# Kernel tuning notes

Hardware: AMD Instinct MI355X
Metric: run time of the kernel (lower is better)

Reference implementation:

```python
import jax, jax.numpy as jnp
import numpy as np

B, S, F = 64, 512, 64      # batch, encoder seq len, input features
H = 512                    # encoder hidden == decoder hidden (required by Attention)
U = 128                    # attention units
T_OUT, OUT_F = 96, 1       # output horizon, output features


def _p(key, shape, scale=0.05):
    return scale * jax.random.normal(key, shape, dtype=jnp.float32)


def setup_inputs() -> dict:
    key = jax.random.key(0)
    ks = jax.random.split(key, 18)
    d = {
        "x": jax.random.normal(ks[0], (B, S, F), dtype=jnp.float32),
        # encoder LSTM (torch gate order i,f,g,o)
        "enc_Wih": _p(ks[1], (4 * H, F)),
        "enc_Whh": _p(ks[2], (4 * H, H)),
        "enc_bih": _p(ks[3], (4 * H,)),
        "enc_bhh": _p(ks[4], (4 * H,)),
        # attention
        "att_W1": _p(ks[5], (U, H)),
        "att_b1": _p(ks[6], (U,)),
        "att_W2": _p(ks[7], (U, H)),
        "att_b2": _p(ks[8], (U,)),
        "att_V": _p(ks[9], (1, U)),
        "att_bV": _p(ks[10], (1,)),
        # decoder LSTM: input = cat(context[H], y_t[OUT_F])
        "dec_Wih": _p(ks[11], (4 * H, H + OUT_F)),
        "dec_Whh": _p(ks[12], (4 * H, H)),
        "dec_bih": _p(ks[13], (4 * H,)),
        "dec_bhh": _p(ks[14], (4 * H,)),
        # output projection
        "out_W": _p(ks[15], (OUT_F, H)),
        "out_b": _p(ks[16], (OUT_F,)),
    }
    return d


def _lstm_gates(pre):
    i, f, g, o = jnp.split(pre, 4, axis=-1)
    return jax.nn.sigmoid(i), jax.nn.sigmoid(f), jnp.tanh(g), jax.nn.sigmoid(o)


def _forward(x, enc_Wih, enc_Whh, enc_bih, enc_bhh,
             att_W1, att_b1, att_W2, att_b2, att_V, att_bV,
             dec_Wih, dec_Whh, dec_bih, dec_bhh, out_W, out_b):
    b = x.shape[0]
    # ---- encoder LSTM over S steps ----
    x_pre = jnp.einsum('bsf,gf->bsg', x, enc_Wih) + enc_bih + enc_bhh  # precompute input GEMM

    def enc_step(carry, xp_t):
        h, c = carry
        i, f, g, o = _lstm_gates(xp_t + h @ enc_Whh.T)
        c = f * c + i * g
        h = o * jnp.tanh(c)
        return (h, c), h

    h0 = jnp.zeros((b, H), x.dtype)
    (enc_hn, _), enc_out = jax.lax.scan(enc_step, (h0, h0), jnp.swapaxes(x_pre, 0, 1))
    enc_out = jnp.swapaxes(enc_out, 0, 1)  # [B,S,H]

    # W2(enc_out) is step-invariant -> hoist out of the decode loop
    w2_enc = jnp.einsum('bsh,uh->bsu', enc_out, att_W2) + att_b2  # [B,S,U]

    # y is None in inference path -> teacher-forcing inputs are zeros
    y_t = jnp.zeros((b, OUT_F), x.dtype)
    dec_bias = dec_bih + dec_bhh  # h0=c0=0 each decoder call (torch code passes no state)

    def dec_step(h_att, _):
        # Bahdanau attention
        w1_h = h_att @ att_W1.T + att_b1                       # [B,U]
        score = jnp.tanh(w1_h[:, None, :] + w2_enc) @ att_V.T + att_bV  # [B,S,1]
        attn = jax.nn.softmax(score, axis=1)
        ctx = jnp.sum(attn * enc_out, axis=1)                  # [B,H]
        # single decoder LSTM cell step from zero state
        x_t = jnp.concatenate([ctx, y_t], axis=-1)             # [B,H+OUT_F]
        i, f, g, o = _lstm_gates(x_t @ dec_Wih.T + dec_bias)   # f*c0 = 0, Whh@h0 = 0
        c = i * g
        h = o * jnp.tanh(c)
        out_t = h @ out_W.T + out_b                            # [B,OUT_F]
        return h, out_t

    _, outs = jax.lax.scan(dec_step, enc_hn, None, length=T_OUT)
    return jnp.swapaxes(outs, 0, 1)  # [B,T_OUT,OUT_F]


def reference(x, enc_Wih, enc_Whh, enc_bih, enc_bhh,
              att_W1, att_b1, att_W2, att_b2, att_V, att_bV,
              dec_Wih, dec_Whh, dec_bih, dec_bhh, out_W, out_b):
    return _forward(x, enc_Wih, enc_Whh, enc_bih, enc_bhh,
                    att_W1, att_b1, att_W2, att_b2, att_V, att_bV,
                    dec_Wih, dec_Whh, dec_bih, dec_bhh, out_W, out_b)
```

## Files before the change

kernel.cpp:

```cpp
#include <hip/hip_runtime.h>

#define Bn 64
#define Sn 512
#define Fn 64
#define Hn 512
#define Un 128
#define Tn 96

typedef __attribute__((ext_vector_type(8))) short bf16x8;
typedef __attribute__((ext_vector_type(4))) float f32x4;

#define MFMA16(a, b, c) __builtin_amdgcn_mfma_f32_16x16x32_bf16(a, b, c, 0, 0, 0)

__device__ __forceinline__ float sigm(float x) { return 1.0f / (1.0f + __expf(-x)); }
__device__ __forceinline__ float tanh_f(float x) {
    x = fminf(fmaxf(x, -15.0f), 15.0f);
    float e = __expf(2.0f * x);
    return (e - 1.0f) / (e + 1.0f);
}
__device__ __forceinline__ short bf16rtn(float f) {
    unsigned u = __float_as_uint(f);
    unsigned r = (u + 0x7FFFu + ((u >> 16) & 1u)) >> 16;
    return (short)r;
}
__device__ __forceinline__ float bf16tof(short s) {
    return __uint_as_float(((unsigned)(unsigned short)s) << 16);
}

__global__ __launch_bounds__(256) void k_split_x(const float* __restrict__ x,
                                                 short* __restrict__ xhi, short* __restrict__ xlo) {
    int t = blockIdx.x * 256 + threadIdx.x;
    int f = t & 63, s = (t >> 6) & 511, b = t >> 15;
    float v = x[t];
    short hi = bf16rtn(v);
    short lo = bf16rtn(v - bf16tof(hi));
    int o = (s * Bn + b) * Fn + f;
    xhi[o] = hi; xlo[o] = lo;
}
__global__ __launch_bounds__(256) void k_split_whh(const float* __restrict__ w,
                                                   short* __restrict__ whi, short* __restrict__ wlo) {
    int t = blockIdx.x * 256 + threadIdx.x;
    int k = t & 511, r = t >> 9;
    int g = r >> 9, j = r & 511;
    float v = w[t];
    short hi = bf16rtn(v);
    short lo = bf16rtn(v - bf16tof(hi));
    int o = (j * 4 + g) * 512 + k;
    whi[o] = hi; wlo[o] = lo;
}
__global__ __launch_bounds__(256) void k_split_wih(const float* __restrict__ w,
                                                   short* __restrict__ whi, short* __restrict__ wlo) {
    int t = blockIdx.x * 256 + threadIdx.x;
    int k = t & 63, r = t >> 6;
    int g = r >> 9, j = r & 511;
    float v = w[t];
    short hi = bf16rtn(v);
    short lo = bf16rtn(v - bf16tof(hi));
    int o = (j * 4 + g) * 64 + k;
    whi[o] = hi; wlo[o] = lo;
}
__global__ __launch_bounds__(256) void k_bias_perm(const float* __restrict__ bih,
                                                   const float* __restrict__ bhh,
                                                   float* __restrict__ bperm) {
    int t = blockIdx.x * 256 + threadIdx.x;
    int g = t >> 9, j = t & 511;
    bperm[j * 4 + g] = bih[t] + bhh[t];
}
__global__ __launch_bounds__(256) void k_w1t(const float* __restrict__ W1, float* __restrict__ W1T) {
    int t = blockIdx.x * 256 + threadIdx.x;
    int u = t >> 9, k = t & 511;
    W1T[k * Un + u] = W1[t];
}
__global__ __launch_bounds__(256) void k_w2t_bf16(const float* __restrict__ W2, short* __restrict__ W2Tb) {
    int t = blockIdx.x * 256 + threadIdx.x;
    int u = t >> 9, j = t & 511;
    W2Tb[j * Un + u] = bf16rtn(W2[t]);
}
__global__ __launch_bounds__(256) void k_transpose_dec(const float* __restrict__ dW, float* __restrict__ WiT,
                                                       float* __restrict__ WgT, float* __restrict__ WoT) {
    int t = blockIdx.x * 256 + threadIdx.x;
    int j = t & 511, j2 = t >> 9;
    WiT[t] = dW[(j)        * 513 + j2];
    WgT[t] = dW[(1024 + j) * 513 + j2];
    WoT[t] = dW[(1536 + j) * 513 + j2];
}
__global__ __launch_bounds__(256) void k_zero_state(float* __restrict__ hz, float* __restrict__ se) {
    int t = blockIdx.x * 256 + threadIdx.x;
    if (t < 98304) hz[t] = 0.0f;
    else se[t - 98304] = 0.0f;
}

__global__ __launch_bounds__(256)
void enc_step_mfma(const short* __restrict__ xhi, const short* __restrict__ xlo,
                   const short* __restrict__ whhHi, const short* __restrict__ whhLo,
                   const short* __restrict__ wihHi, const short* __restrict__ wihLo,
                   const float* __restrict__ bperm,
                   const short* __restrict__ hHiP, const short* __restrict__ hLoP,
                   short* __restrict__ hHiN, short* __restrict__ hLoN,
                   float* __restrict__ cstG, short* __restrict__ encJ, int t)
{
    const int blk = blockIdx.x;
    const int jt = blk >> 2, bt = blk & 3;
    const int tid = threadIdx.x;
    const int wv = tid >> 6, l = tid & 63;
    const int lr = l & 15, lk = l >> 4;
    const int row  = jt * 16 + lr;
    const int bcol = bt * 16 + lr;

    f32x4 acc0 = {0.f, 0.f, 0.f, 0.f};
    f32x4 acc1 = {0.f, 0.f, 0.f, 0.f};
    #pragma unroll
    for (int c = 0; c < 4; c++) {
        int k0 = wv * 128 + c * 32 + lk * 8;
        bf16x8 Ah = *(const bf16x8*)(whhHi + row * 512 + k0);
        bf16x8 Al = *(const bf16x8*)(whhLo + row * 512 + k0);
        bf16x8 Bh = *(const bf16x8*)(hHiP + bcol * 512 + k0);
        bf16x8 Bl = *(const bf16x8*)(hLoP + bcol * 512 + k0);
        if (c & 1) {
            acc1 = MFMA16(Ah, Bh, acc1);
            acc1 = MFMA16(Ah, Bl, acc1);
            acc1 = MFMA16(Al, Bh, acc1);
        } else {
            acc0 = MFMA16(Ah, Bh, acc0);
            acc0 = MFMA16(Ah, Bl, acc0);
            acc0 = MFMA16(Al, Bh, acc0);
        }
    }
    if (wv < 2) {
        int k0 = wv * 32 + lk * 8;
        bf16x8 Ah = *(const bf16x8*)(wihHi + row * 64 + k0);
        bf16x8 Al = *(const bf16x8*)(wihLo + row * 64 + k0);
        bf16x8 Bh = *(const bf16x8*)(xhi + ((size_t)t * 64 + bcol) * 64 + k0);
        bf16x8 Bl = *(const bf16x8*)(xlo + ((size_t)t * 64 + bcol) * 64 + k0);
        acc0 = MFMA16(Ah, Bh, acc0);
        acc1 = MFMA16(Ah, Bl, acc1);
        acc0 = MFMA16(Al, Bh, acc0);
    }
    f32x4 acc = acc0 + acc1;

    __shared__ float red[3][64][4];
    if (wv) *(f32x4*)(&red[wv - 1][l][0]) = acc;
    __syncthreads();
    if (wv == 0) {
        const int jloc = jt * 4 + lk;
        const f32x4 bias = *(const f32x4*)(bperm + jt * 16 + lk * 4);
        f32x4 r0 = *(const f32x4*)(&red[0][l][0]);
        f32x4 r1 = *(const f32x4*)(&red[1][l][0]);
        f32x4 r2 = *(const f32x4*)(&red[2][l][0]);
        float pi = acc[0] + r0[0] + r1[0] + r2[0] + bias[0];
        float pf = acc[1] + r0[1] + r1[1] + r2[1] + bias[1];
        float pg = acc[2] + r0[2] + r1[2] + r2[2] + bias[2];
        float po = acc[3] + r0[3] + r1[3] + r2[3] + bias[3];
        float ig = sigm(pi), fg = sigm(pf), gg = tanh_f(pg), og = sigm(po);
        float cn = fg * cstG[jloc * Bn + bcol] + ig * gg;
        float hv = og * tanh_f(cn);
        cstG[jloc * Bn + bcol] = cn;
        short hi16 = bf16rtn(hv);
        short lo16 = bf16rtn(hv - bf16tof(hi16));
        hHiN[bcol * 512 + jloc] = hi16;
        hLoN[bcol * 512 + jloc] = lo16;
        encJ[jloc * (Sn * Bn) + t * Bn + bcol] = hi16;
    }
}

__global__ __launch_bounds__(256)
void w2enc_k(const short* __restrict__ encJ, const short* __restrict__ W2Tb,
             const float* __restrict__ b2, short* __restrict__ w2eb)
{
    __shared__ float tile[64 * 64];
    const int s = blockIdx.x;
    const int tid = threadIdx.x;
    const int u = tid & 127, bq = tid >> 7;
    float acc[32];
    #pragma unroll
    for (int i = 0; i < 32; i++) acc[i] = 0.f;
    for (int jc = 0; jc < 8; jc++) {
        __syncthreads();
        #pragma unroll
        for (int r = 0; r < 16; r++) {
            int e = r * 256 + tid;
            int jl = e >> 6, b = e & 63;
            tile[e] = bf16tof(encJ[(jc * 64 + jl) * (Sn * Bn) + s * Bn + b]);
        }
        __syncthreads();
        for (int jl = 0; jl < 64; jl++) {
            float wv = bf16tof(W2Tb[(jc * 64 + jl) * Un + u]);
            const float4* trow = (const float4*)&tile[jl * 64 + bq * 32];
            #pragma unroll
            for (int i = 0; i < 8; i++) {
                float4 t4 = trow[i];
                acc[i*4+0] += t4.x * wv; acc[i*4+1] += t4.y * wv;
                acc[i*4+2] += t4.z * wv; acc[i*4+3] += t4.w * wv;
            }
        }
    }
    float bb = b2[u];
    #pragma unroll
    for (int i = 0; i < 32; i++)
        w2eb[(((size_t)(bq * 32 + i)) * Sn + s) * Un + u] = bf16rtn(acc[i] + bb);
}

__global__ __launch_bounds__(256)
void dec_attn_k(const float* __restrict__ hdec, const short* __restrict__ encJ,
                const float* __restrict__ W1T, const float* __restrict__ b1,
                const float* __restrict__ Vv, const float* __restrict__ bV,
                const short* __restrict__ w2eb, const float* __restrict__ oW,
                const float* __restrict__ ob, float* __restrict__ eT,
                float* __restrict__ sumE, float* __restrict__ out, int t)
{
    __shared__ float hs[512];
    __shared__ float w1h[Un];
    __shared__ float Vs[Un];
    __shared__ float red2[256];
    const int tid = threadIdx.x;
    const int b = blockIdx.x >> 2, sc = blockIdx.x & 3;

    if (t == 0) {
        hs[tid]       = bf16tof(encJ[tid * (Sn * Bn) + (Sn - 1) * Bn + b]);
        hs[tid + 256] = bf16tof(encJ[(tid + 256) * (Sn * Bn) + (Sn - 1) * Bn + b]);
    } else {
        hs[tid]       = hdec[tid * Bn + b];
        hs[tid + 256] = hdec[(tid + 256) * Bn + b];
    }
    if (tid < 128) Vs[tid] = Vv[tid];
    __syncthreads();

    if (sc == 0 && t > 0) {
        red2[tid] = oW[tid] * hs[tid] + oW[tid + 256] * hs[tid + 256];
        __syncthreads();
        for (int w = 128; w > 0; w >>= 1) { if (tid < w) red2[tid] += red2[tid + w]; __syncthreads(); }
        if (tid == 0) out[b * Tn + (t - 1)] = red2[0] + ob[0];
        __syncthreads();
    }

    {
        const int u = tid & 127, kh = tid >> 7;
        float a = 0.f;
        #pragma unroll 8
        for (int k = 0; k < 256; k++) {
            int kk = kh * 256 + k;
            a += W1T[kk * Un + u] * hs[kk];
        }
        red2[tid] = a;
    }
    __syncthreads();
    if (tid < 128) w1h[tid] = red2[tid] + red2[tid + 128] + b1[tid];
    __syncthreads();

    const int sl = sc * 128 + (tid >> 1), uh = tid & 1;
    const short* r  = w2eb + ((size_t)b * Sn + sl) * Un + uh * 64;
    const float* wp = w1h + uh * 64;
    const float* vp = Vs + uh * 64;
    float s0 = 0.f;
    #pragma unroll 4
    for (int u2 = 0; u2 < 64; u2++) s0 += vp[u2] * tanh_f(wp[u2] + bf16tof(r[u2]));
    s0 += __shfl_xor(s0, 1);
    float e = 0.f;
    if (uh == 0) {
        e = __expf(s0 + bV[0]);
        eT[sl * Bn + b] = e;
    }
    __syncthreads();
    red2[tid] = e;
    __syncthreads();
    for (int w = 128; w > 0; w >>= 1) { if (tid < w) red2[tid] += red2[tid + w]; __syncthreads(); }
    if (tid == 0) atomicAdd(&sumE[t * Bn + b], red2[0]);
}

__global__ __launch_bounds__(256)
void dec_ctx_k(const float* __restrict__ eT, const short* __restrict__ encJ,
               float* __restrict__ ctx)
{
    const int tid = threadIdx.x;
    const int j = blockIdx.x;
    const int b = tid & 63, sq = tid >> 6;
    const short* ep = encJ + j * (Sn * Bn) + b;
    float a = 0.f;
    #pragma unroll 8
    for (int s = sq * 128; s < sq * 128 + 128; s++)
        a += eT[s * Bn + b] * bf16tof(ep[s * Bn]);
    __shared__ float red[256];
    red[tid] = a;
    __syncthreads();
    if (sq == 0) ctx[j * Bn + b] = red[b] + red[64 + b] + red[128 + b] + red[192 + b];
}

__global__ __launch_bounds__(256)
void dec_gate_k(const float* __restrict__ ctx, const float* __restrict__ sumE,
                const float* __restrict__ WiT, const float* __restrict__ WgT,
                const float* __restrict__ WoT, const float* __restrict__ dbih,
                const float* __restrict__ dbhh, float* __restrict__ hdec, int t)
{
    const int tid = threadIdx.x;
    const int b = tid & 63, kq = tid >> 6;
    const int j = blockIdx.x;
    float ai = 0.f, ag = 0.f, ao = 0.f;
    #pragma unroll 4
    for (int k = kq * 128; k < kq * 128 + 128; k++) {
        float cv = ctx[k * Bn + b];
        ai += WiT[k * Hn + j] * cv;
        ag += WgT[k * Hn + j] * cv;
        ao += WoT[k * Hn + j] * cv;
    }
    __shared__ float red[3][4][64];
    red[0][kq][b] = ai; red[1][kq][b] = ag; red[2][kq][b] = ao;
    __syncthreads();
    if (kq == 0) {
        float inv = 1.0f / sumE[t * Bn + b];
        float pi = (red[0][0][b] + red[0][1][b] + red[0][2][b] + red[0][3][b]) * inv + dbih[j] + dbhh[j];
        float pg = (red[1][0][b] + red[1][1][b] + red[1][2][b] + red[1][3][b]) * inv + dbih[2*Hn + j] + dbhh[2*Hn + j];
        float po = (red[2][0][b] + red[2][1][b] + red[2][2][b] + red[2][3][b]) * inv + dbih[3*Hn + j] + dbhh[3*Hn + j];
        float cc = sigm(pi) * tanh_f(pg);
        float hh = sigm(po) * tanh_f(cc);
        hdec[j * Bn + b] = hh;
    }
}

__global__ __launch_bounds__(64)
void dec_out_k(const float* __restrict__ hdec, const float* __restrict__ oW,
               const float* __restrict__ ob, float* __restrict__ out, int t)
{
    const int b = blockIdx.x;
    const int tid = threadIdx.x;
    float a = 0.f;
    #pragma unroll
    for (int q = 0; q < 8; q++) {
        int j = tid + q * 64;
        a += oW[j] * hdec[j * Bn + b];
    }
    for (int off = 32; off; off >>= 1) a += __shfl_down(a, off, 64);
    if (tid == 0) out[b * Tn + t] = a + ob[0];
}

extern "C" void kernel_launch(void* const* d_in, const int* in_sizes, int n_in,
                              void* d_out, int out_size, void* d_ws, size_t ws_size,
                              hipStream_t stream) {
    const float* x    = (const float*)d_in[0];
    const float* eWih = (const float*)d_in[1];
    const float* eWhh = (const float*)d_in[2];
    const float* ebih = (const float*)d_in[3];
    const float* ebhh = (const float*)d_in[4];
    const float* aW1  = (const float*)d_in[5];
    const float* ab1  = (const float*)d_in[6];
    const float* aW2  = (const float*)d_in[7];
    const float* ab2  = (const float*)d_in[8];
    const float* aV   = (const float*)d_in[9];
    const float* abV  = (const float*)d_in[10];
    const float* dWih = (const float*)d_in[11];
    const float* dbih = (const float*)d_in[13];
    const float* dbhh = (const float*)d_in[14];
    const float* oW   = (const float*)d_in[15];
    const float* ob   = (const float*)d_in[16];
    float* out = (float*)d_out;

    char* wsb = (char*)d_ws;
    short* xhi    = (short*)(wsb + 0);
    short* xlo    = (short*)(wsb + 4194304);
    short* whhHi  = (short*)(wsb + 8388608);
    short* whhLo  = (short*)(wsb + 10485760);
    short* wihHi  = (short*)(wsb + 12582912);
    short* wihLo  = (short*)(wsb + 12845056);
    float* bperm  = (float*)(wsb + 13107200);
    short* W2Tb   = (short*)(wsb + 13115392);
    float* W1T    = (float*)(wsb + 13246464);
    float* WiT    = (float*)(wsb + 13508608);
    float* WgT    = (float*)(wsb + 14557184);
    float* WoT    = (float*)(wsb + 15605760);
    short* hHi    = (short*)(wsb + 16654336);
    short* hLo    = (short*)(wsb + 16785408);
    float* cstG   = (float*)(wsb + 16916480);
    short* encJ   = (short*)(wsb + 17047552);
    short* w2eb   = (short*)(wsb + 50601984);
    float* eT     = (float*)(wsb + 58990592);
    float* sumE   = (float*)(wsb + 59121664);
    float* ctx    = (float*)(wsb + 59146240);
    float* hdec   = (float*)(wsb + 59277312);

    k_split_x      <<<8192, 256, 0, stream>>>(x, xhi, xlo);
    k_split_whh    <<<4096, 256, 0, stream>>>(eWhh, whhHi, whhLo);
    k_split_wih    <<<512,  256, 0, stream>>>(eWih, wihHi, wihLo);
    k_bias_perm    <<<8,    256, 0, stream>>>(ebih, ebhh, bperm);
    k_w1t          <<<256,  256, 0, stream>>>(aW1, W1T);
    k_w2t_bf16     <<<256,  256, 0, stream>>>(aW2, W2Tb);
    k_transpose_dec<<<1024, 256, 0, stream>>>(dWih, WiT, WgT, WoT);
    k_zero_state   <<<408,  256, 0, stream>>>((float*)hHi, sumE);

    for (int t = 0; t < Sn; t++) {
        const int pr = t & 1, pw = 1 - pr;
        enc_step_mfma<<<512, 256, 0, stream>>>(xhi, xlo, whhHi, whhLo, wihHi, wihLo,
                                               bperm,
                                               hHi + pr * 32768, hLo + pr * 32768,
                                               hHi + pw * 32768, hLo + pw * 32768,
                                               cstG, encJ, t);
    }

    w2enc_k<<<512, 256, 0, stream>>>(encJ, W2Tb, ab2, w2eb);

    for (int t = 0; t < Tn; t++) {
        dec_attn_k<<<256, 256, 0, stream>>>(hdec, encJ, W1T, ab1, aV, abV, w2eb,
                                            oW, ob, eT, sumE, out, t);
        dec_ctx_k <<<512, 256, 0, stream>>>(eT, encJ, ctx);
        dec_gate_k<<<512, 256, 0, stream>>>(ctx, sumE, WiT, WgT, WoT, dbih, dbhh, hdec, t);
    }
    dec_out_k<<<64, 64, 0, stream>>>(hdec, oW, ob, out, Tn - 1);
}
```

Before: 7.694 ms.

## Fuse encoder time loop into persistent kernel with global atomic barrier

Replaces 512 per-timestep encoder kernel launches with one persistent kernel that loops over time, keeping Whh/Wih fragments and cell state in registers. Steps are separated by a grid-wide barrier built from spread atomic counters with spin-waiting, and the hi/lo bf16 hidden halves are packed into one u32 so each element is exchanged with a single relaxed atomic store. This removes launch overhead and repeated weight reloads, but it depends on all 512 blocks being co-resident (launch bounds 256,2) and on relaxed atomics giving correct visibility; spin latency could also dominate.

```diff
diff --git a/kernel.cpp b/kernel.cpp
--- a/kernel.cpp
+++ b/kernel.cpp
@@ -9,6 +9,8 @@
 
 typedef __attribute__((ext_vector_type(8))) short bf16x8;
 typedef __attribute__((ext_vector_type(4))) float f32x4;
+typedef unsigned int u32;
+typedef unsigned long long u64;
 
 #define MFMA16(a, b, c) __builtin_amdgcn_mfma_f32_16x16x32_bf16(a, b, c, 0, 0, 0)
 
@@ -84,20 +86,19 @@
     WgT[t] = dW[(1024 + j) * 513 + j2];
     WoT[t] = dW[(1536 + j) * 513 + j2];
 }
-__global__ __launch_bounds__(256) void k_zero_state(float* __restrict__ hz, float* __restrict__ se) {
-    int t = blockIdx.x * 256 + threadIdx.x;
-    if (t < 98304) hz[t] = 0.0f;
-    else se[t - 98304] = 0.0f;
-}
-
-__global__ __launch_bounds__(256)
-void enc_step_mfma(const short* __restrict__ xhi, const short* __restrict__ xlo,
-                   const short* __restrict__ whhHi, const short* __restrict__ whhLo,
-                   const short* __restrict__ wihHi, const short* __restrict__ wihLo,
-                   const float* __restrict__ bperm,
-                   const short* __restrict__ hHiP, const short* __restrict__ hLoP,
-                   short* __restrict__ hHiN, short* __restrict__ hLoN,
-                   float* __restrict__ cstG, short* __restrict__ encJ, int t)
+__global__ __launch_bounds__(256) void k_zero_state(u32* __restrict__ z, float* __restrict__ se) {
+    int t = blockIdx.x * 256 + threadIdx.x;
+    if (t < 131072) z[t] = 0u;
+    else se[t - 131072] = 0.0f;
+}
+
+__global__ __launch_bounds__(256, 2)
+void enc_persist2(const short* __restrict__ xhi, const short* __restrict__ xlo,
+                  const short* __restrict__ whhHi, const short* __restrict__ whhLo,
+                  const short* __restrict__ wihHi, const short* __restrict__ wihLo,
+                  const float* __restrict__ bperm,
+                  u32* __restrict__ hPk, u32* __restrict__ ctrs,
+                  short* __restrict__ encJ)
 {
     const int blk = blockIdx.x;
     const int jt = blk >> 2, bt = blk & 3;
@@ -107,59 +108,104 @@
     const int row  = jt * 16 + lr;
     const int bcol = bt * 16 + lr;
 
-    f32x4 acc0 = {0.f, 0.f, 0.f, 0.f};
-    f32x4 acc1 = {0.f, 0.f, 0.f, 0.f};
+    bf16x8 Ahi[4], Alo[4];
     #pragma unroll
     for (int c = 0; c < 4; c++) {
         int k0 = wv * 128 + c * 32 + lk * 8;
-        bf16x8 Ah = *(const bf16x8*)(whhHi + row * 512 + k0);
-        bf16x8 Al = *(const bf16x8*)(whhLo + row * 512 + k0);
-        bf16x8 Bh = *(const bf16x8*)(hHiP + bcol * 512 + k0);
-        bf16x8 Bl = *(const bf16x8*)(hLoP + bcol * 512 + k0);
-        if (c & 1) {
-            acc1 = MFMA16(Ah, Bh, acc1);
-            acc1 = MFMA16(Ah, Bl, acc1);
-            acc1 = MFMA16(Al, Bh, acc1);
-        } else {
-            acc0 = MFMA16(Ah, Bh, acc0);
-            acc0 = MFMA16(Ah, Bl, acc0);
-            acc0 = MFMA16(Al, Bh, acc0);
-        }
-    }
+        Ahi[c] = *(const bf16x8*)(whhHi + row * 512 + k0);
+        Alo[c] = *(const bf16x8*)(whhLo + row * 512 + k0);
+    }
+    bf16x8 AXhi = {}, AXlo = {};
     if (wv < 2) {
         int k0 = wv * 32 + lk * 8;
-        bf16x8 Ah = *(const bf16x8*)(wihHi + row * 64 + k0);
-        bf16x8 Al = *(const bf16x8*)(wihLo + row * 64 + k0);
-        bf16x8 Bh = *(const bf16x8*)(xhi + ((size_t)t * 64 + bcol) * 64 + k0);
-        bf16x8 Bl = *(const bf16x8*)(xlo + ((size_t)t * 64 + bcol) * 64 + k0);
-        acc0 = MFMA16(Ah, Bh, acc0);
-        acc1 = MFMA16(Ah, Bl, acc1);
-        acc0 = MFMA16(Al, Bh, acc0);
-    }
-    f32x4 acc = acc0 + acc1;
+        AXhi = *(const bf16x8*)(wihHi + row * 64 + k0);
+        AXlo = *(const bf16x8*)(wihLo + row * 64 + k0);
+    }
+    const int jloc = jt * 4 + lk;
+    const int bV   = bt * 16 + lr;
+    const f32x4 bias = *(const f32x4*)(bperm + jt * 16 + lk * 4);
+    float cst = 0.0f;
 
     __shared__ float red[3][64][4];
-    if (wv) *(f32x4*)(&red[wv - 1][l][0]) = acc;
-    __syncthreads();
-    if (wv == 0) {
-        const int jloc = jt * 4 + lk;
-        const f32x4 bias = *(const f32x4*)(bperm + jt * 16 + lk * 4);
-        f32x4 r0 = *(const f32x4*)(&red[0][l][0]);
-        f32x4 r1 = *(const f32x4*)(&red[1][l][0]);
-        f32x4 r2 = *(const f32x4*)(&red[2][l][0]);
-        float pi = acc[0] + r0[0] + r1[0] + r2[0] + bias[0];
-        float pf = acc[1] + r0[1] + r1[1] + r2[1] + bias[1];
-        float pg = acc[2] + r0[2] + r1[2] + r2[2] + bias[2];
-        float po = acc[3] + r0[3] + r1[3] + r2[3] + bias[3];
-        float ig = sigm(pi), fg = sigm(pf), gg = tanh_f(pg), og = sigm(po);
-        float cn = fg * cstG[jloc * Bn + bcol] + ig * gg;
-        float hv = og * tanh_f(cn);
-        cstG[jloc * Bn + bcol] = cn;
-        short hi16 = bf16rtn(hv);
-        short lo16 = bf16rtn(hv - bf16tof(hi16));
-        hHiN[bcol * 512 + jloc] = hi16;
-        hLoN[bcol * 512 + jloc] = lo16;
-        encJ[jloc * (Sn * Bn) + t * Bn + bcol] = hi16;
+
+    #pragma unroll 1
+    for (int t = 0; t < 512; t++) {
+        const int pr = t & 1;
+        const u32* hp = hPk + pr * 32768 + bcol * 512;
+        f32x4 acc0 = {0.f, 0.f, 0.f, 0.f};
+        f32x4 acc1 = {0.f, 0.f, 0.f, 0.f};
+        #pragma unroll
+        for (int c = 0; c < 4; c++) {
+            int k0 = wv * 128 + c * 32 + lk * 8;
+            const u64* q = (const u64*)(hp + k0);
+            union { u64 q[4]; u32 d[8]; } u;
+            u.q[0] = __hip_atomic_load(q + 0, __ATOMIC_RELAXED, __HIP_MEMORY_SCOPE_AGENT);
+            u.q[1] = __hip_atomic_load(q + 1, __ATOMIC_RELAXED, __HIP_MEMORY_SCOPE_AGENT);
+            u.q[2] = __hip_atomic_load(q + 2, __ATOMIC_RELAXED, __HIP_MEMORY_SCOPE_AGENT);
+            u.q[3] = __hip_atomic_load(q + 3, __ATOMIC_RELAXED, __HIP_MEMORY_SCOPE_AGENT);
+            union { bf16x8 v; u32 d[4]; } Bh, Bl;
+            #pragma unroll
+            for (int i = 0; i < 4; i++) {
+                u32 a = u.d[2 * i], b = u.d[2 * i + 1];
+                Bh.d[i] = (a >> 16) | (b & 0xFFFF0000u);
+                Bl.d[i] = (a & 0xFFFFu) | (b << 16);
+            }
+            if (c & 1) {
+                acc1 = MFMA16(Ahi[c], Bh.v, acc1);
+                acc1 = MFMA16(Ahi[c], Bl.v, acc1);
+                acc1 = MFMA16(Alo[c], Bh.v, acc1);
+            } else {
+                acc0 = MFMA16(Ahi[c], Bh.v, acc0);
+                acc0 = MFMA16(Ahi[c], Bl.v, acc0);
+                acc0 = MFMA16(Alo[c], Bh.v, acc0);
+            }
+        }
+        if (wv < 2) {
+            int k0 = wv * 32 + lk * 8;
+            bf16x8 Bh = *(const bf16x8*)(xhi + ((size_t)t * 64 + bcol) * 64 + k0);
+            bf16x8 Bl = *(const bf16x8*)(xlo + ((size_t)t * 64 + bcol) * 64 + k0);
+            acc0 = MFMA16(AXhi, Bh, acc0);
+            acc1 = MFMA16(AXhi, Bl, acc1);
+            acc0 = MFMA16(AXlo, Bh, acc0);
+        }
+        f32x4 acc = acc0 + acc1;
+
+        if (wv) *(f32x4*)(&red[wv - 1][l][0]) = acc;
+        __syncthreads();
+        if (wv == 0) {
+            f32x4 r0 = *(const f32x4*)(&red[0][l][0]);
+            f32x4 r1 = *(const f32x4*)(&red[1][l][0]);
+            f32x4 r2 = *(const f32x4*)(&red[2][l][0]);
+            float pi = acc[0] + r0[0] + r1[0] + r2[0] + bias[0];
+            float pf = acc[1] + r0[1] + r1[1] + r2[1] + bias[1];
+            float pg = acc[2] + r0[2] + r1[2] + r2[2] + bias[2];
+            float po = acc[3] + r0[3] + r1[3] + r2[3] + bias[3];
+            float ig = sigm(pi), fg = sigm(pf), gg = tanh_f(pg), og = sigm(po);
+            cst = fg * cst + ig * gg;
+            float hv = og * tanh_f(cst);
+            short hi16 = bf16rtn(hv);
+            short lo16 = bf16rtn(hv - bf16tof(hi16));
+            u32 pk = ((u32)(unsigned short)hi16 << 16) | (u32)(unsigned short)lo16;
+            __hip_atomic_store(hPk + (1 - pr) * 32768 + bV * 512 + jloc, pk,
+                               __ATOMIC_RELAXED, __HIP_MEMORY_SCOPE_AGENT);
+            encJ[jloc * (Sn * Bn) + t * Bn + bV] = hi16;
+        }
+        asm volatile("s_waitcnt vmcnt(0)" ::: "memory");
+        if (tid == 0) {
+            u32* cb = ctrs + t * 128;
+            __hip_atomic_fetch_add(cb + (blk & 7) * 16, 1u,
+                                   __ATOMIC_RELAXED, __HIP_MEMORY_SCOPE_AGENT);
+            u32 sum;
+            do {
+                sum = 0u;
+                #pragma unroll
+                for (int i = 0; i < 8; i++)
+                    sum += __hip_atomic_load(cb + i * 16, __ATOMIC_RELAXED,
+                                             __HIP_MEMORY_SCOPE_AGENT);
+                if (sum < 512u) __builtin_amdgcn_s_sleep(1);
+            } while (sum < 512u);
+        }
+        __syncthreads();
     }
 }
 
@@ -366,15 +412,14 @@
     float* WiT    = (float*)(wsb + 13508608);
     float* WgT    = (float*)(wsb + 14557184);
     float* WoT    = (float*)(wsb + 15605760);
-    short* hHi    = (short*)(wsb + 16654336);
-    short* hLo    = (short*)(wsb + 16785408);
-    float* cstG   = (float*)(wsb + 16916480);
-    short* encJ   = (short*)(wsb + 17047552);
-    short* w2eb   = (short*)(wsb + 50601984);
-    float* eT     = (float*)(wsb + 58990592);
-    float* sumE   = (float*)(wsb + 59121664);
-    float* ctx    = (float*)(wsb + 59146240);
-    float* hdec   = (float*)(wsb + 59277312);
+    u32*   hPk    = (u32*)  (wsb + 16654336);
+    u32*   ctrs   = (u32*)  (wsb + 16916480);
+    short* encJ   = (short*)(wsb + 17178624);
+    short* w2eb   = (short*)(wsb + 50733056);
+    float* eT     = (float*)(wsb + 59121664);
+    float* sumE   = (float*)(wsb + 59252736);
+    float* ctx    = (float*)(wsb + 59277312);
+    float* hdec   = (float*)(wsb + 59408384);
 
     k_split_x      <<<8192, 256, 0, stream>>>(x, xhi, xlo);
     k_split_whh    <<<4096, 256, 0, stream>>>(eWhh, whhHi, whhLo);
@@ -383,16 +428,10 @@
     k_w1t          <<<256,  256, 0, stream>>>(aW1, W1T);
     k_w2t_bf16     <<<256,  256, 0, stream>>>(aW2, W2Tb);
     k_transpose_dec<<<1024, 256, 0, stream>>>(dWih, WiT, WgT, WoT);
-    k_zero_state   <<<408,  256, 0, stream>>>((float*)hHi, sumE);
-
-    for (int t = 0; t < Sn; t++) {
-        const int pr = t & 1, pw = 1 - pr;
-        enc_step_mfma<<<512, 256, 0, stream>>>(xhi, xlo, whhHi, whhLo, wihHi, wihLo,
-                                               bperm,
-                                               hHi + pr * 32768, hLo + pr * 32768,
-                                               hHi + pw * 32768, hLo + pw * 32768,
-                                               cstG, encJ, t);
-    }
+    k_zero_state   <<<536,  256, 0, stream>>>(hPk, sumE);
+
+    enc_persist2<<<512, 256, 0, stream>>>(xhi, xlo, whhHi, whhLo, wihHi, wihLo,
+                                          bperm, hPk, ctrs, encJ);
 
     w2enc_k<<<512, 256, 0, stream>>>(encJ, W2Tb, ab2, w2eb);
 
```

New measurement: 11.75 ms. 1.53x slower.

## Replace per-step encoder launches with persistent kernel using global flag barrier

Applied to the files above, without the earlier changes.

Swaps the 512 per-timestep encoder kernel launches for a single persistent 32-block kernel. Each block owns 64 gate rows, keeps its cell state in registers and reads packed hi/lo hidden state through agent-scope atomic loads into LDS. Blocks then synchronize across steps with a spin-wait flag barrier, which removes launch overhead and the cross-wave LDS reduction. It also vectorizes the bf16 loads in the attention score loop. The cost is that only 32 CUs are used, each block re-reads its weight rows every step, and the design depends on all blocks being co-resident and on relaxed-atomic visibility being correct.

```diff
diff --git a/kernel.cpp b/kernel.cpp
--- a/kernel.cpp
+++ b/kernel.cpp
@@ -9,8 +9,11 @@
 
 typedef __attribute__((ext_vector_type(8))) short bf16x8;
 typedef __attribute__((ext_vector_type(4))) float f32x4;
+typedef unsigned int u32;
+typedef unsigned long long u64;
 
 #define MFMA16(a, b, c) __builtin_amdgcn_mfma_f32_16x16x32_bf16(a, b, c, 0, 0, 0)
+#define ALOAD64(p) __hip_atomic_load((p), __ATOMIC_RELAXED, __HIP_MEMORY_SCOPE_AGENT)
 
 __device__ __forceinline__ float sigm(float x) { return 1.0f / (1.0f + __expf(-x)); }
 __device__ __forceinline__ float tanh_f(float x) {
@@ -84,82 +87,158 @@
     WgT[t] = dW[(1024 + j) * 513 + j2];
     WoT[t] = dW[(1536 + j) * 513 + j2];
 }
-__global__ __launch_bounds__(256) void k_zero_state(float* __restrict__ hz, float* __restrict__ se) {
-    int t = blockIdx.x * 256 + threadIdx.x;
-    if (t < 98304) hz[t] = 0.0f;
-    else se[t - 98304] = 0.0f;
-}
-
-__global__ __launch_bounds__(256)
-void enc_step_mfma(const short* __restrict__ xhi, const short* __restrict__ xlo,
-                   const short* __restrict__ whhHi, const short* __restrict__ whhLo,
-                   const short* __restrict__ wihHi, const short* __restrict__ wihLo,
-                   const float* __restrict__ bperm,
-                   const short* __restrict__ hHiP, const short* __restrict__ hLoP,
-                   short* __restrict__ hHiN, short* __restrict__ hLoN,
-                   float* __restrict__ cstG, short* __restrict__ encJ, int t)
-{
+__global__ __launch_bounds__(256) void k_zero_state(u32* __restrict__ z, float* __restrict__ se) {
+    int t = blockIdx.x * 256 + threadIdx.x;
+    if (t < 66048) z[t] = 0u;
+    else se[t - 66048] = 0.0f;
+}
+
+__global__ __launch_bounds__(256, 1)
+void enc_persist3(const short* __restrict__ xhi, const short* __restrict__ xlo,
+                  const short* __restrict__ whhHi, const short* __restrict__ whhLo,
+                  const short* __restrict__ wihHi, const short* __restrict__ wihLo,
+                  const float* __restrict__ bperm,
+                  u32* __restrict__ hPk, u32* __restrict__ flags,
+                  short* __restrict__ encJ)
+{
+    __shared__ short hiL[64 * 520];
+    __shared__ short loL[64 * 520];
     const int blk = blockIdx.x;
-    const int jt = blk >> 2, bt = blk & 3;
     const int tid = threadIdx.x;
     const int wv = tid >> 6, l = tid & 63;
     const int lr = l & 15, lk = l >> 4;
-    const int row  = jt * 16 + lr;
-    const int bcol = bt * 16 + lr;
-
-    f32x4 acc0 = {0.f, 0.f, 0.f, 0.f};
-    f32x4 acc1 = {0.f, 0.f, 0.f, 0.f};
+    const int rtB = (wv >> 1) * 32;
+    const int ctB = (wv & 1) * 32;
+    const int r0 = blk * 64 + rtB + lr;
+    const int r1 = r0 + 16;
+    const int b0 = ctB + lr, b1 = b0 + 16;
+
+    bf16x8 XA[2][2][2];
     #pragma unroll
-    for (int c = 0; c < 4; c++) {
-        int k0 = wv * 128 + c * 32 + lk * 8;
-        bf16x8 Ah = *(const bf16x8*)(whhHi + row * 512 + k0);
-        bf16x8 Al = *(const bf16x8*)(whhLo + row * 512 + k0);
-        bf16x8 Bh = *(const bf16x8*)(hHiP + bcol * 512 + k0);
-        bf16x8 Bl = *(const bf16x8*)(hLoP + bcol * 512 + k0);
-        if (c & 1) {
-            acc1 = MFMA16(Ah, Bh, acc1);
-            acc1 = MFMA16(Ah, Bl, acc1);
-            acc1 = MFMA16(Al, Bh, acc1);
-        } else {
-            acc0 = MFMA16(Ah, Bh, acc0);
-            acc0 = MFMA16(Ah, Bl, acc0);
-            acc0 = MFMA16(Al, Bh, acc0);
-        }
-    }
-    if (wv < 2) {
-        int k0 = wv * 32 + lk * 8;
-        bf16x8 Ah = *(const bf16x8*)(wihHi + row * 64 + k0);
-        bf16x8 Al = *(const bf16x8*)(wihLo + row * 64 + k0);
-        bf16x8 Bh = *(const bf16x8*)(xhi + ((size_t)t * 64 + bcol) * 64 + k0);
-        bf16x8 Bl = *(const bf16x8*)(xlo + ((size_t)t * 64 + bcol) * 64 + k0);
-        acc0 = MFMA16(Ah, Bh, acc0);
-        acc1 = MFMA16(Ah, Bl, acc1);
-        acc0 = MFMA16(Al, Bh, acc0);
-    }
-    f32x4 acc = acc0 + acc1;
-
-    __shared__ float red[3][64][4];
-    if (wv) *(f32x4*)(&red[wv - 1][l][0]) = acc;
-    __syncthreads();
-    if (wv == 0) {
-        const int jloc = jt * 4 + lk;
-        const f32x4 bias = *(const f32x4*)(bperm + jt * 16 + lk * 4);
-        f32x4 r0 = *(const f32x4*)(&red[0][l][0]);
-        f32x4 r1 = *(const f32x4*)(&red[1][l][0]);
-        f32x4 r2 = *(const f32x4*)(&red[2][l][0]);
-        float pi = acc[0] + r0[0] + r1[0] + r2[0] + bias[0];
-        float pf = acc[1] + r0[1] + r1[1] + r2[1] + bias[1];
-        float pg = acc[2] + r0[2] + r1[2] + r2[2] + bias[2];
-        float po = acc[3] + r0[3] + r1[3] + r2[3] + bias[3];
-        float ig = sigm(pi), fg = sigm(pf), gg = tanh_f(pg), og = sigm(po);
-        float cn = fg * cstG[jloc * Bn + bcol] + ig * gg;
-        float hv = og * tanh_f(cn);
-        cstG[jloc * Bn + bcol] = cn;
-        short hi16 = bf16rtn(hv);
-        short lo16 = bf16rtn(hv - bf16tof(hi16));
-        hHiN[bcol * 512 + jloc] = hi16;
-        hLoN[bcol * 512 + jloc] = lo16;
-        encJ[jloc * (Sn * Bn) + t * Bn + bcol] = hi16;
+    for (int cw = 0; cw < 2; cw++) {
+        int k0 = cw * 32 + lk * 8;
+        XA[cw][0][0] = *(const bf16x8*)(wihHi + r0 * 64 + k0);
+        XA[cw][0][1] = *(const bf16x8*)(wihLo + r0 * 64 + k0);
+        XA[cw][1][0] = *(const bf16x8*)(wihHi + r1 * 64 + k0);
+        XA[cw][1][1] = *(const bf16x8*)(wihLo + r1 * 64 + k0);
+    }
+    const f32x4 bias0 = *(const f32x4*)(bperm + blk * 64 + rtB + lk * 4);
+    const f32x4 bias1 = *(const f32x4*)(bperm + blk * 64 + rtB + 16 + lk * 4);
+    float cst[2][2] = {{0.f, 0.f}, {0.f, 0.f}};
+
+    #pragma unroll 1
+    for (int t = 0; t < 512; t++) {
+        const int pr = t & 1;
+        bf16x8 XB[2][2][2];
+        #pragma unroll
+        for (int cw = 0; cw < 2; cw++) {
+            int k0 = cw * 32 + lk * 8;
+            XB[cw][0][0] = *(const bf16x8*)(xhi + ((size_t)t * 64 + b0) * 64 + k0);
+            XB[cw][0][1] = *(const bf16x8*)(xlo + ((size_t)t * 64 + b0) * 64 + k0);
+            XB[cw][1][0] = *(const bf16x8*)(xhi + ((size_t)t * 64 + b1) * 64 + k0);
+            XB[cw][1][1] = *(const bf16x8*)(xlo + ((size_t)t * 64 + b1) * 64 + k0);
+        }
+        {
+            const u32* src = hPk + pr * 32768;
+            #pragma unroll 4
+            for (int i = 0; i < 16; i++) {
+                int idx = i * 2048 + tid * 8;
+                const u64* q = (const u64*)(src + idx);
+                u64 q0 = ALOAD64(q + 0);
+                u64 q1 = ALOAD64(q + 1);
+                u64 q2 = ALOAD64(q + 2);
+                u64 q3 = ALOAD64(q + 3);
+                u32 d0 = (u32)q0, d1 = (u32)(q0 >> 32);
+                u32 d2 = (u32)q1, d3 = (u32)(q1 >> 32);
+                u32 d4 = (u32)q2, d5 = (u32)(q2 >> 32);
+                u32 d6 = (u32)q3, d7 = (u32)(q3 >> 32);
+                union { bf16x8 v; u32 d[4]; } H, L;
+                H.d[0] = (d0 >> 16) | (d1 & 0xFFFF0000u);
+                L.d[0] = (d0 & 0xFFFFu) | (d1 << 16);
+                H.d[1] = (d2 >> 16) | (d3 & 0xFFFF0000u);
+                L.d[1] = (d2 & 0xFFFFu) | (d3 << 16);
+                H.d[2] = (d4 >> 16) | (d5 & 0xFFFF0000u);
+                L.d[2] = (d4 & 0xFFFFu) | (d5 << 16);
+                H.d[3] = (d6 >> 16) | (d7 & 0xFFFF0000u);
+                L.d[3] = (d6 & 0xFFFFu) | (d7 << 16);
+                int bb = idx >> 9, kk = idx & 511;
+                *(bf16x8*)(&hiL[bb * 520 + kk]) = H.v;
+                *(bf16x8*)(&loL[bb * 520 + kk]) = L.v;
+            }
+        }
+        __syncthreads();
+        f32x4 a00 = {0.f,0.f,0.f,0.f}, a01 = {0.f,0.f,0.f,0.f};
+        f32x4 a10 = {0.f,0.f,0.f,0.f}, a11 = {0.f,0.f,0.f,0.f};
+        #pragma unroll 4
+        for (int c = 0; c < 16; c++) {
+            int k0 = c * 32 + lk * 8;
+            bf16x8 Ah0 = *(const bf16x8*)(whhHi + (size_t)r0 * 512 + k0);
+            bf16x8 Al0 = *(const bf16x8*)(whhLo + (size_t)r0 * 512 + k0);
+            bf16x8 Ah1 = *(const bf16x8*)(whhHi + (size_t)r1 * 512 + k0);
+            bf16x8 Al1 = *(const bf16x8*)(whhLo + (size_t)r1 * 512 + k0);
+            bf16x8 Bh0 = *(const bf16x8*)(&hiL[b0 * 520 + k0]);
+            bf16x8 Bl0 = *(const bf16x8*)(&loL[b0 * 520 + k0]);
+            bf16x8 Bh1 = *(const bf16x8*)(&hiL[b1 * 520 + k0]);
+            bf16x8 Bl1 = *(const bf16x8*)(&loL[b1 * 520 + k0]);
+            a00 = MFMA16(Ah0, Bh0, a00); a00 = MFMA16(Ah0, Bl0, a00); a00 = MFMA16(Al0, Bh0, a00);
+            a01 = MFMA16(Ah0, Bh1, a01); a01 = MFMA16(Ah0, Bl1, a01); a01 = MFMA16(Al0, Bh1, a01);
+            a10 = MFMA16(Ah1, Bh0, a10); a10 = MFMA16(Ah1, Bl0, a10); a10 = MFMA16(Al1, Bh0, a10);
+            a11 = MFMA16(Ah1, Bh1, a11); a11 = MFMA16(Ah1, Bl1, a11); a11 = MFMA16(Al1, Bh1, a11);
+        }
+        #pragma unroll
+        for (int cw = 0; cw < 2; cw++) {
+            a00 = MFMA16(XA[cw][0][0], XB[cw][0][0], a00);
+            a00 = MFMA16(XA[cw][0][0], XB[cw][0][1], a00);
+            a00 = MFMA16(XA[cw][0][1], XB[cw][0][0], a00);
+            a01 = MFMA16(XA[cw][0][0], XB[cw][1][0], a01);
+            a01 = MFMA16(XA[cw][0][0], XB[cw][1][1], a01);
+            a01 = MFMA16(XA[cw][0][1], XB[cw][1][0], a01);
+            a10 = MFMA16(XA[cw][1][0], XB[cw][0][0], a10);
+            a10 = MFMA16(XA[cw][1][0], XB[cw][0][1], a10);
+            a10 = MFMA16(XA[cw][1][1], XB[cw][0][0], a10);
+            a11 = MFMA16(XA[cw][1][0], XB[cw][1][0], a11);
+            a11 = MFMA16(XA[cw][1][0], XB[cw][1][1], a11);
+            a11 = MFMA16(XA[cw][1][1], XB[cw][1][0], a11);
+        }
+        const int pw = 1 - pr;
+        #pragma unroll
+        for (int i = 0; i < 2; i++) {
+            #pragma unroll
+            for (int j = 0; j < 2; j++) {
+                f32x4 A = (i == 0) ? ((j == 0) ? a00 : a01) : ((j == 0) ? a10 : a11);
+                f32x4 bs = (i == 0) ? bias0 : bias1;
+                float pi = A[0] + bs[0];
+                float pf = A[1] + bs[1];
+                float pg = A[2] + bs[2];
+                float po = A[3] + bs[3];
+                float ig = sigm(pi), fg = sigm(pf), gg = tanh_f(pg), og = sigm(po);
+                float cn = fg * cst[i][j] + ig * gg;
+                cst[i][j] = cn;
+                float hv = og * tanh_f(cn);
+                short hi16 = bf16rtn(hv);
+                short lo16 = bf16rtn(hv - bf16tof(hi16));
+                u32 pk = ((u32)(unsigned short)hi16 << 16) | (u32)(unsigned short)lo16;
+                int jg = blk * 16 + (wv >> 1) * 8 + i * 4 + lk;
+                int bb = ctB + j * 16 + lr;
+                __hip_atomic_store(hPk + pw * 32768 + bb * 512 + jg, pk,
+                                   __ATOMIC_RELAXED, __HIP_MEMORY_SCOPE_AGENT);
+                encJ[(size_t)jg * (Sn * Bn) + t * 64 + bb] = hi16;
+            }
+        }
+        __syncthreads();
+        if (tid == 0)
+            __hip_atomic_store(&flags[blk * 16], (u32)(t + 1),
+                               __ATOMIC_RELAXED, __HIP_MEMORY_SCOPE_AGENT);
+        if (wv == 0) {
+            while (true) {
+                u32 v = (l < 32) ? __hip_atomic_load(&flags[l * 16], __ATOMIC_RELAXED,
+                                                     __HIP_MEMORY_SCOPE_AGENT)
+                                 : 0xFFFFFFFFu;
+                if (__all(v > (u32)t)) break;
+                __builtin_amdgcn_s_sleep(2);
+            }
+        }
+        __syncthreads();
     }
 }
 
@@ -252,8 +331,13 @@
     const float* wp = w1h + uh * 64;
     const float* vp = Vs + uh * 64;
     float s0 = 0.f;
-    #pragma unroll 4
-    for (int u2 = 0; u2 < 64; u2++) s0 += vp[u2] * tanh_f(wp[u2] + bf16tof(r[u2]));
+    #pragma unroll
+    for (int q = 0; q < 8; q++) {
+        bf16x8 v8 = *(const bf16x8*)(r + q * 8);
+        #pragma unroll
+        for (int e2 = 0; e2 < 8; e2++)
+            s0 += vp[q * 8 + e2] * tanh_f(wp[q * 8 + e2] + bf16tof(v8[e2]));
+    }
     s0 += __shfl_xor(s0, 1);
     float e = 0.f;
     if (uh == 0) {
@@ -366,15 +450,14 @@
     float* WiT    = (float*)(wsb + 13508608);
     float* WgT    = (float*)(wsb + 14557184);
     float* WoT    = (float*)(wsb + 15605760);
-    short* hHi    = (short*)(wsb + 16654336);
-    short* hLo    = (short*)(wsb + 16785408);
-    float* cstG   = (float*)(wsb + 16916480);
-    short* encJ   = (short*)(wsb + 17047552);
-    short* w2eb   = (short*)(wsb + 50601984);
-    float* eT     = (float*)(wsb + 58990592);
-    float* sumE   = (float*)(wsb + 59121664);
-    float* ctx    = (float*)(wsb + 59146240);
-    float* hdec   = (float*)(wsb + 59277312);
+    u32*   hPk    = (u32*)  (wsb + 16654336);
+    u32*   flags  = (u32*)  (wsb + 16916480);
+    short* encJ   = (short*)(wsb + 16918528);
+    short* w2eb   = (short*)(wsb + 50472960);
+    float* eT     = (float*)(wsb + 58861568);
+    float* sumE   = (float*)(wsb + 58992640);
+    float* ctx    = (float*)(wsb + 59017216);
+    float* hdec   = (float*)(wsb + 59148288);
 
     k_split_x      <<<8192, 256, 0, stream>>>(x, xhi, xlo);
     k_split_whh    <<<4096, 256, 0, stream>>>(eWhh, whhHi, whhLo);
@@ -383,16 +466,10 @@
     k_w1t          <<<256,  256, 0, stream>>>(aW1, W1T);
     k_w2t_bf16     <<<256,  256, 0, stream>>>(aW2, W2Tb);
     k_transpose_dec<<<1024, 256, 0, stream>>>(dWih, WiT, WgT, WoT);
-    k_zero_state   <<<408,  256, 0, stream>>>((float*)hHi, sumE);
-
-    for (int t = 0; t < Sn; t++) {
-        const int pr = t & 1, pw = 1 - pr;
-        enc_step_mfma<<<512, 256, 0, stream>>>(xhi, xlo, whhHi, whhLo, wihHi, wihLo,
-                                               bperm,
-                                               hHi + pr * 32768, hLo + pr * 32768,
-                                               hHi + pw * 32768, hLo + pw * 32768,
-                                               cstG, encJ, t);
-    }
+    k_zero_state   <<<282,  256, 0, stream>>>(hPk, sumE);
+
+    enc_persist3<<<32, 256, 0, stream>>>(xhi, xlo, whhHi, whhLo, wihHi, wihLo,
+                                         bperm, hPk, flags, encJ);
 
     w2enc_k<<<512, 256, 0, stream>>>(encJ, W2Tb, ab2, w2eb);
 
```

Result: slower. 11.94 ms (+55.2%).

## Restructure encoder step to one block per gate tile with full-K per wave

Applied to the files above, without the earlier changes.

The encoder step kernel drops from 512 blocks, where each block split K across four waves and reduced through shared memory, to 128 blocks where each wave owns a 16-column batch tile and runs the full K=512 loop itself. This removes the shared-memory reduction and the __syncthreads, and each block loads the Whh row tile once for all four batch tiles. The cost is a longer serial MFMA chain per wave with a single accumulator and fewer blocks on the GPU. The attention score loop also switches to vectorized 8-wide bf16 loads of the w2enc row.

```diff
diff --git a/kernel.cpp b/kernel.cpp
--- a/kernel.cpp
+++ b/kernel.cpp
@@ -9,6 +9,7 @@
 
 typedef __attribute__((ext_vector_type(8))) short bf16x8;
 typedef __attribute__((ext_vector_type(4))) float f32x4;
+typedef unsigned int u32;
 
 #define MFMA16(a, b, c) __builtin_amdgcn_mfma_f32_16x16x32_bf16(a, b, c, 0, 0, 0)
 
@@ -91,76 +92,66 @@
 }
 
 __global__ __launch_bounds__(256)
-void enc_step_mfma(const short* __restrict__ xhi, const short* __restrict__ xlo,
-                   const short* __restrict__ whhHi, const short* __restrict__ whhLo,
-                   const short* __restrict__ wihHi, const short* __restrict__ wihLo,
-                   const float* __restrict__ bperm,
-                   const short* __restrict__ hHiP, const short* __restrict__ hLoP,
-                   short* __restrict__ hHiN, short* __restrict__ hLoN,
-                   float* __restrict__ cstG, short* __restrict__ encJ, int t)
-{
-    const int blk = blockIdx.x;
-    const int jt = blk >> 2, bt = blk & 3;
+void enc_step2(const short* __restrict__ xhi, const short* __restrict__ xlo,
+               const short* __restrict__ whhHi, const short* __restrict__ whhLo,
+               const short* __restrict__ wihHi, const short* __restrict__ wihLo,
+               const float* __restrict__ bperm,
+               const short* __restrict__ hHiP, const short* __restrict__ hLoP,
+               short* __restrict__ hHiN, short* __restrict__ hLoN,
+               float* __restrict__ cstG, short* __restrict__ encJ, int t)
+{
+    const int jt = blockIdx.x;
     const int tid = threadIdx.x;
     const int wv = tid >> 6, l = tid & 63;
     const int lr = l & 15, lk = l >> 4;
     const int row  = jt * 16 + lr;
-    const int bcol = bt * 16 + lr;
-
-    f32x4 acc0 = {0.f, 0.f, 0.f, 0.f};
-    f32x4 acc1 = {0.f, 0.f, 0.f, 0.f};
-    #pragma unroll
-    for (int c = 0; c < 4; c++) {
-        int k0 = wv * 128 + c * 32 + lk * 8;
-        bf16x8 Ah = *(const bf16x8*)(whhHi + row * 512 + k0);
-        bf16x8 Al = *(const bf16x8*)(whhLo + row * 512 + k0);
-        bf16x8 Bh = *(const bf16x8*)(hHiP + bcol * 512 + k0);
-        bf16x8 Bl = *(const bf16x8*)(hLoP + bcol * 512 + k0);
-        if (c & 1) {
-            acc1 = MFMA16(Ah, Bh, acc1);
-            acc1 = MFMA16(Ah, Bl, acc1);
-            acc1 = MFMA16(Al, Bh, acc1);
-        } else {
-            acc0 = MFMA16(Ah, Bh, acc0);
-            acc0 = MFMA16(Ah, Bl, acc0);
-            acc0 = MFMA16(Al, Bh, acc0);
+    const int bcol = wv * 16 + lr;
+
+    f32x4 acc = {0.f, 0.f, 0.f, 0.f};
+    {
+        bf16x8 XB[2][2];
+        #pragma unroll
+        for (int cw = 0; cw < 2; cw++) {
+            int k0 = cw * 32 + lk * 8;
+            XB[cw][0] = *(const bf16x8*)(xhi + ((size_t)t * 64 + bcol) * 64 + k0);
+            XB[cw][1] = *(const bf16x8*)(xlo + ((size_t)t * 64 + bcol) * 64 + k0);
         }
-    }
-    if (wv < 2) {
-        int k0 = wv * 32 + lk * 8;
-        bf16x8 Ah = *(const bf16x8*)(wihHi + row * 64 + k0);
-        bf16x8 Al = *(const bf16x8*)(wihLo + row * 64 + k0);
-        bf16x8 Bh = *(const bf16x8*)(xhi + ((size_t)t * 64 + bcol) * 64 + k0);
-        bf16x8 Bl = *(const bf16x8*)(xlo + ((size_t)t * 64 + bcol) * 64 + k0);
-        acc0 = MFMA16(Ah, Bh, acc0);
-        acc1 = MFMA16(Ah, Bl, acc1);
-        acc0 = MFMA16(Al, Bh, acc0);
-    }
-    f32x4 acc = acc0 + acc1;
-
-    __shared__ float red[3][64][4];
-    if (wv) *(f32x4*)(&red[wv - 1][l][0]) = acc;
-    __syncthreads();
-    if (wv == 0) {
-        const int jloc = jt * 4 + lk;
-        const f32x4 bias = *(const f32x4*)(bperm + jt * 16 + lk * 4);
-        f32x4 r0 = *(const f32x4*)(&red[0][l][0]);
-        f32x4 r1 = *(const f32x4*)(&red[1][l][0]);
-        f32x4 r2 = *(const f32x4*)(&red[2][l][0]);
-        float pi = acc[0] + r0[0] + r1[0] + r2[0] + bias[0];
-        float pf = acc[1] + r0[1] + r1[1] + r2[1] + bias[1];
-        float pg = acc[2] + r0[2] + r1[2] + r2[2] + bias[2];
-        float po = acc[3] + r0[3] + r1[3] + r2[3] + bias[3];
-        float ig = sigm(pi), fg = sigm(pf), gg = tanh_f(pg), og = sigm(po);
-        float cn = fg * cstG[jloc * Bn + bcol] + ig * gg;
-        float hv = og * tanh_f(cn);
-        cstG[jloc * Bn + bcol] = cn;
-        short hi16 = bf16rtn(hv);
-        short lo16 = bf16rtn(hv - bf16tof(hi16));
-        hHiN[bcol * 512 + jloc] = hi16;
-        hLoN[bcol * 512 + jloc] = lo16;
-        encJ[jloc * (Sn * Bn) + t * Bn + bcol] = hi16;
-    }
+        #pragma unroll
+        for (int cw = 0; cw < 2; cw++) {
+            int k0 = cw * 32 + lk * 8;
+            bf16x8 Ah = *(const bf16x8*)(wihHi + (size_t)row * 64 + k0);
+            bf16x8 Al = *(const bf16x8*)(wihLo + (size_t)row * 64 + k0);
+            acc = MFMA16(Ah, XB[cw][0], acc);
+            acc = MFMA16(Ah, XB[cw][1], acc);
+            acc = MFMA16(Al, XB[cw][0], acc);
+        }
+    }
+    #pragma unroll 4
+    for (int c = 0; c < 16; c++) {
+        int k0 = c * 32 + lk * 8;
+        bf16x8 Ah = *(const bf16x8*)(whhHi + (size_t)row * 512 + k0);
+        bf16x8 Al = *(const bf16x8*)(whhLo + (size_t)row * 512 + k0);
+        bf16x8 Bh = *(const bf16x8*)(hHiP + (size_t)bcol * 512 + k0);
+        bf16x8 Bl = *(const bf16x8*)(hLoP + (size_t)bcol * 512 + k0);
+        acc = MFMA16(Ah, Bh, acc);
+        acc = MFMA16(Ah, Bl, acc);
+        acc = MFMA16(Al, Bh, acc);
+    }
+    const int jloc = jt * 4 + lk;
+    const f32x4 bias = *(const f32x4*)(bperm + jt * 16 + lk * 4);
+    float pi = acc[0] + bias[0];
+    float pf = acc[1] + bias[1];
+    float pg = acc[2] + bias[2];
+    float po = acc[3] + bias[3];
+    float ig = sigm(pi), fg = sigm(pf), gg = tanh_f(pg), og = sigm(po);
+    float cn = fg * cstG[jloc * Bn + bcol] + ig * gg;
+    float hv = og * tanh_f(cn);
+    cstG[jloc * Bn + bcol] = cn;
+    short hi16 = bf16rtn(hv);
+    short lo16 = bf16rtn(hv - bf16tof(hi16));
+    hHiN[bcol * 512 + jloc] = hi16;
+    hLoN[bcol * 512 + jloc] = lo16;
+    encJ[(size_t)jloc * (Sn * Bn) + t * Bn + bcol] = hi16;
 }
 
 __global__ __launch_bounds__(256)
@@ -252,8 +243,13 @@
     const float* wp = w1h + uh * 64;
     const float* vp = Vs + uh * 64;
     float s0 = 0.f;
-    #pragma unroll 4
-    for (int u2 = 0; u2 < 64; u2++) s0 += vp[u2] * tanh_f(wp[u2] + bf16tof(r[u2]));
+    #pragma unroll
+    for (int q = 0; q < 8; q++) {
+        bf16x8 v8 = *(const bf16x8*)(r + q * 8);
+        #pragma unroll
+        for (int e2 = 0; e2 < 8; e2++)
+            s0 += vp[q * 8 + e2] * tanh_f(wp[q * 8 + e2] + bf16tof(v8[e2]));
+    }
     s0 += __shfl_xor(s0, 1);
     float e = 0.f;
     if (uh == 0) {
@@ -387,11 +383,11 @@
 
     for (int t = 0; t < Sn; t++) {
         const int pr = t & 1, pw = 1 - pr;
-        enc_step_mfma<<<512, 256, 0, stream>>>(xhi, xlo, whhHi, whhLo, wihHi, wihLo,
-                                               bperm,
-                                               hHi + pr * 32768, hLo + pr * 32768,
-                                               hHi + pw * 32768, hLo + pw * 32768,
-                                               cstG, encJ, t);
+        enc_step2<<<128, 256, 0, stream>>>(xhi, xlo, whhHi, whhLo, wihHi, wihLo,
+                                           bperm,
+                                           hHi + pr * 32768, hLo + pr * 32768,
+                                           hHi + pw * 32768, hLo + pw * 32768,
+                                           cstG, encJ, t);
     }
 
     w2enc_k<<<512, 256, 0, stream>>>(encJ, W2Tb, ab2, w2eb);
```

Result: slower. 9.844 ms (+27.9%).
